# Kernel tuning notes

Hardware: AMD Instinct MI355X
Metric: run time of the kernel (lower is better)

The kernel has to match this reference:

```python
import jax, jax.numpy as jnp
import numpy as np

FREQ_BANDS = 10
LN_EPS = 1e-5


def nerf_positional_encoding(x, L=FREQ_BANDS):
    # x: (..., 3) -> (..., 3*2*L). Per-frequency [sin(2^i x), cos(2^i x)].
    freqs = 2.0 ** jnp.arange(L, dtype=x.dtype)            # (L,)
    xb = x[..., None, :] * freqs[:, None]                  # (..., L, 3)
    enc = jnp.concatenate([jnp.sin(xb), jnp.cos(xb)], -1)  # (..., L, 6)
    return enc.reshape(x.shape[:-1] + (L * 6,))


def farthest_point_sampling(xyz, npoint):
    # xyz: (B, N, 3) -> (B, npoint) int32. Deterministic start at index 0
    # (torch version uses a random start; start choice is arbitrary for FPS).
    B, N, _ = xyz.shape
    binds = jnp.arange(B)

    def step(carry, _):
        dist, far = carry
        c = xyz[binds, far]                                # (B, 3)
        d = jnp.sum((xyz - c[:, None, :]) ** 2, axis=-1)   # (B, N)
        dist = jnp.minimum(dist, d)
        nxt = jnp.argmax(dist, axis=-1).astype(jnp.int32)
        return (dist, nxt), far

    init = (jnp.full((B, N), 1e10, xyz.dtype), jnp.zeros((B,), jnp.int32))
    _, idx = jax.lax.scan(step, init, None, length=npoint)
    return jnp.swapaxes(idx, 0, 1)                         # (B, npoint)


def _layernorm(x, g, b):
    m = jnp.mean(x, axis=-1, keepdims=True)
    v = jnp.var(x, axis=-1, keepdims=True)
    return (x - m) * jax.lax.rsqrt(v + LN_EPS) * g + b


def setup_inputs() -> dict:
    key = jax.random.key(0)
    ks = jax.random.split(key, 8)
    B, N, C = 8, 16384, 64
    d_in = C + 3 * 2 * FREQ_BANDS                          # 124
    dims = [d_in, 128, 128, 256]

    def lin(k, din, dout):
        return jax.random.normal(k, (din, dout), jnp.float32) / np.sqrt(din)

    return {
        "xyz": jax.random.normal(ks[0], (B, N, 3), jnp.float32),
        "features": jax.random.normal(ks[1], (B, N, C), jnp.float32),
        "W1": lin(ks[2], dims[0], dims[1]), "b1": jnp.zeros((dims[1],), jnp.float32),
        "g1": jnp.ones((dims[1],), jnp.float32), "be1": jnp.zeros((dims[1],), jnp.float32),
        "W2": lin(ks[3], dims[1], dims[2]), "b2": jnp.zeros((dims[2],), jnp.float32),
        "g2": jnp.ones((dims[2],), jnp.float32), "be2": jnp.zeros((dims[2],), jnp.float32),
        "W3": lin(ks[4], dims[2], dims[3]), "b3": jnp.zeros((dims[3],), jnp.float32),
        "npoint": 2048,
        "nsample": 32,
    }


def reference(xyz, features, W1, b1, g1, be1, W2, b2, g2, be2, W3, b3, npoint, nsample):
    # FPS centroids
    fps_idx = farthest_point_sampling(xyz, npoint)                 # (B, S)
    new_xyz = jnp.take_along_axis(xyz, fps_idx[..., None], axis=1) # (B, S, 3)

    # KNN: squared distances preserve topk ordering of cdist
    d2 = jnp.sum((new_xyz[:, :, None, :] - xyz[:, None, :, :]) ** 2, axis=-1)  # (B,S,N)
    _, knn_idx = jax.lax.top_k(-d2, nsample)                        # (B, S, k)

    gather = jax.vmap(lambda pts, idx: pts[idx])                    # (N,D),(S,k)->(S,k,D)
    grouped_xyz = gather(xyz, knn_idx)                              # (B, S, k, 3)
    rel_pos = grouped_xyz - new_xyz[:, :, None, :]
    rel_enc = nerf_positional_encoding(rel_pos)                     # (B, S, k, 60)

    grouped_feat = gather(features, knn_idx)                        # (B, S, k, C)
    h = jnp.concatenate([grouped_feat, rel_enc], axis=-1)           # (B, S, k, C+60)

    h = jax.nn.relu(_layernorm(h @ W1 + b1, g1, be1))
    h = jax.nn.relu(_layernorm(h @ W2 + b2, g2, be2))
    h = h @ W3 + b3                                                 # (B, S, k, 256)
    new_features = jnp.max(h, axis=2)                               # (B, S, 256)
    return new_xyz, new_features
```

## Files before the change

kernel.cpp:

```cpp
#include <hip/hip_runtime.h>
#include <cstdint>
#include <cstddef>

#define BATCH   8
#define NPTS    16384
#define CFEAT   64
#define NPOINT  2048
#define NSAMPLE 32
#define DIN     124
#define D1      128
#define D2      128
#define D3      256
#define LN_EPS  1e-5f

#define NFPS      8
#define NBLOCKS   256
#define KNN_ITEMS 128
#define MLP_ITEMS 2048
#define TOT_ITEMS (KNN_ITEMS + MLP_ITEMS)

#define SB_BYTES   19872
#define SMEM_BYTES (8 * SB_BYTES)

#define CTL_QHEAD   0
#define CTL_PROG    1024
#define CTL_KCNT    4096
#define CTL_KFLAG   16384
#define CTL_BYTES   32768

#define PTS16(F) F(0) F(1) F(2) F(3) F(4) F(5) F(6) F(7) \
                 F(8) F(9) F(10) F(11) F(12) F(13) F(14) F(15)

__device__ float          g_sx[BATCH][NPTS];
__device__ float          g_sy[BATCH][NPTS];
__device__ float          g_sz[BATCH][NPTS];
__device__ unsigned short g_so[BATCH][NPTS];

__attribute__((amdgpu_waves_per_eu(4, 4)))
__global__ __launch_bounds__(1024) void fused_kernel(
    const float* __restrict__ xyz, const float* __restrict__ features,
    const float* __restrict__ W1, const float* __restrict__ b1,
    const float* __restrict__ g1, const float* __restrict__ be1,
    const float* __restrict__ W2, const float* __restrict__ b2,
    const float* __restrict__ g2, const float* __restrict__ be2,
    const float* __restrict__ W3, const float* __restrict__ b3,
    int* __restrict__ knn_idx, unsigned char* __restrict__ ctl,
    float* __restrict__ new_xyz, float* __restrict__ out)
{
  __shared__ __align__(16) unsigned char smem[SMEM_BYTES];
  __shared__ unsigned s_item;
  const int t = threadIdx.x;

  unsigned* qhead = (unsigned*)(ctl + CTL_QHEAD);
#define PROG_AT(b)  ((int*)(ctl + CTL_PROG + (b) * 256))
#define KCNT_AT(k)  ((unsigned*)(ctl + CTL_KCNT + (k) * 64))
#define KFLAG_AT(k) ((unsigned*)(ctl + CTL_KFLAG + (k) * 64))

  if (blockIdx.x < NFPS) {
    const int b = blockIdx.x;
    const float* X = xyz + (size_t)b * NPTS * 3;

    float4 (*s_mind4)[1024] = reinterpret_cast<float4(*)[1024]>(smem);
    unsigned short* s_oidx  = (unsigned short*)(smem + 65536);
    float* wvv              = (float*)(smem + 98304);
    unsigned long long* s_packed = (unsigned long long*)(smem + 98368);
    float (*wbb)[6]         = (float(*)[6])(smem + 98496);
    float* gpar             = (float*)(smem + 98944);
    unsigned* cstart        = (unsigned*)(smem + 99008);
    unsigned* ccur          = (unsigned*)(smem + 101120);
    float (*redbuf)[6]      = (float(*)[6])(smem + 103168);

#define DECLP(i) float px##i, py##i, pz##i;
    PTS16(DECLP)
#undef DECLP
#define LOADP(i) { int j = t + (i << 10);  \
    px##i = X[3 * j + 0];                  \
    py##i = X[3 * j + 1];                  \
    pz##i = X[3 * j + 2]; }
    PTS16(LOADP)
#undef LOADP

    {
      float mnx = px0, mxx = px0, mny = py0, mxy = py0, mnz = pz0, mxz = pz0;
#define BB(i) { mnx = fminf(mnx, px##i); mxx = fmaxf(mxx, px##i);  \
                mny = fminf(mny, py##i); mxy = fmaxf(mxy, py##i);  \
                mnz = fminf(mnz, pz##i); mxz = fmaxf(mxz, pz##i); }
      PTS16(BB)
#undef BB
#pragma unroll
      for (int off = 32; off >= 1; off >>= 1) {
        mnx = fminf(mnx, __shfl_xor(mnx, off)); mxx = fmaxf(mxx, __shfl_xor(mxx, off));
        mny = fminf(mny, __shfl_xor(mny, off)); mxy = fmaxf(mxy, __shfl_xor(mxy, off));
        mnz = fminf(mnz, __shfl_xor(mnz, off)); mxz = fmaxf(mxz, __shfl_xor(mxz, off));
      }
      if ((t & 63) == 0) {
        int w = t >> 6;
        redbuf[w][0] = mnx; redbuf[w][1] = mxx; redbuf[w][2] = mny;
        redbuf[w][3] = mxy; redbuf[w][4] = mnz; redbuf[w][5] = mxz;
      }
      if (t < 513) cstart[t] = 0;
      __syncthreads();
      if (t == 0) {
        float a0 = redbuf[0][0], a1 = redbuf[0][1], a2 = redbuf[0][2];
        float a3 = redbuf[0][3], a4 = redbuf[0][4], a5 = redbuf[0][5];
        for (int w = 1; w < 16; ++w) {
          a0 = fminf(a0, redbuf[w][0]); a1 = fmaxf(a1, redbuf[w][1]);
          a2 = fminf(a2, redbuf[w][2]); a3 = fmaxf(a3, redbuf[w][3]);
          a4 = fminf(a4, redbuf[w][4]); a5 = fmaxf(a5, redbuf[w][5]);
        }
        float rx = a1 - a0, ry = a3 - a2, rz = a5 - a4;
        gpar[0] = a0; gpar[1] = a2; gpar[2] = a4;
        gpar[3] = (rx > 1e-20f) ? 8.0f / rx : 0.f;
        gpar[4] = (ry > 1e-20f) ? 8.0f / ry : 0.f;
        gpar[5] = (rz > 1e-20f) ? 8.0f / rz : 0.f;
        s_packed[0] = 0ull; s_packed[1] = 0ull;
      }
      __syncthreads();
    }

#define CELLM(x, y, z) ({                                              \
    int ix_ = (int)((x - gpar[0]) * gpar[3]);                          \
    int iy_ = (int)((y - gpar[1]) * gpar[4]);                          \
    int iz_ = (int)((z - gpar[2]) * gpar[5]);                          \
    ix_ = ix_ < 0 ? 0 : (ix_ > 7 ? 7 : ix_);                           \
    iy_ = iy_ < 0 ? 0 : (iy_ > 7 ? 7 : iy_);                           \
    iz_ = iz_ < 0 ? 0 : (iz_ > 7 ? 7 : iz_);                           \
    (((ix_ & 1) | ((ix_ & 2) << 2) | ((ix_ & 4) << 4))                 \
     | (((iy_ & 1) | ((iy_ & 2) << 2) | ((iy_ & 4) << 4)) << 1)        \
     | (((iz_ & 1) | ((iz_ & 2) << 2) | ((iz_ & 4) << 4)) << 2)); })

#define CIDK(i) { int m_ = CELLM(px##i, py##i, pz##i); \
    atomicAdd(&cstart[m_ + 1], 1u); }
    PTS16(CIDK)
#undef CIDK
    __syncthreads();

    if (t < 64) {
      unsigned v[8], p[8];
      unsigned run = 0;
#pragma unroll
      for (int j = 0; j < 8; ++j) { v[j] = cstart[t * 8 + 1 + j]; run += v[j]; p[j] = run; }
      unsigned tot = run;
#pragma unroll
      for (int off = 1; off < 64; off <<= 1) {
        unsigned u = __shfl_up(run, off);
        if ((t & 63) >= off) run += u;
      }
      unsigned excl = run - tot;
      if (t == 0) cstart[0] = 0;
#pragma unroll
      for (int j = 0; j < 8; ++j) cstart[t * 8 + 1 + j] = excl + p[j];
    }
    __syncthreads();
    if (t < 512) ccur[t] = cstart[t];
    __syncthreads();

#define SCATK(i) { int j = t + (i << 10);                              \
    int m_ = CELLM(px##i, py##i, pz##i);                               \
    unsigned dst = atomicAdd(&ccur[m_], 1u);                           \
    g_sx[b][dst] = px##i; g_sy[b][dst] = py##i; g_sz[b][dst] = pz##i;  \
    g_so[b][dst] = (unsigned short)j; }
    PTS16(SCATK)
#undef SCATK
#undef CELLM
    __syncthreads();

    float tlx = 1e30f, thx = -1e30f, tly = 1e30f, thy = -1e30f,
          tlz = 1e30f, thz = -1e30f;
#define RELK(i) { int p_ = (t << 4) + i;                               \
    px##i = g_sx[b][p_]; py##i = g_sy[b][p_]; pz##i = g_sz[b][p_];     \
    s_oidx[(i << 10) + t] = g_so[b][p_];                               \
    tlx = fminf(tlx, px##i); thx = fmaxf(thx, px##i);                  \
    tly = fminf(tly, py##i); thy = fmaxf(thy, py##i);                  \
    tlz = fminf(tlz, pz##i); thz = fmaxf(thz, pz##i); }
    PTS16(RELK)
#undef RELK
    s_mind4[0][t] = make_float4(1e10f, 1e10f, 1e10f, 1e10f);
    s_mind4[1][t] = make_float4(1e10f, 1e10f, 1e10f, 1e10f);
    s_mind4[2][t] = make_float4(1e10f, 1e10f, 1e10f, 1e10f);
    s_mind4[3][t] = make_float4(1e10f, 1e10f, 1e10f, 1e10f);

#pragma unroll
    for (int off = 32; off >= 1; off >>= 1) {
      tlx = fminf(tlx, __shfl_xor(tlx, off)); thx = fmaxf(thx, __shfl_xor(thx, off));
      tly = fminf(tly, __shfl_xor(tly, off)); thy = fmaxf(thy, __shfl_xor(thy, off));
      tlz = fminf(tlz, __shfl_xor(tlz, off)); thz = fmaxf(thz, __shfl_xor(thz, off));
    }
    if ((t & 63) == 0) {
      int w = t >> 6;
      wbb[w][0] = tlx; wbb[w][1] = thx; wbb[w][2] = tly;
      wbb[w][3] = thy; wbb[w][4] = tlz; wbb[w][5] = thz;
    }

    float mybest = -1.0f;
    float wvmax  = 1e10f;
    float cx = X[0], cy = X[1], cz = X[2];
    __syncthreads();

    for (int s = 0; s < NPOINT; ++s) {
      if (t == 0) {
        float* o = new_xyz + ((size_t)b * NPOINT + s) * 3;
        o[0] = cx; o[1] = cy; o[2] = cz;
        if (((s + 1) & 15) == 0) {
          __builtin_amdgcn_fence(__ATOMIC_RELEASE, "agent");
          __hip_atomic_store(PROG_AT(b), s + 1, __ATOMIC_RELAXED,
                             __HIP_MEMORY_SCOPE_AGENT);
        }
      }
      if (s == NPOINT - 1) break;

      asm volatile("" : "+v"(px0), "+v"(px1), "+v"(px2), "+v"(px3),
                        "+v"(px4), "+v"(px5), "+v"(px6), "+v"(px7),
                        "+v"(px8), "+v"(px9), "+v"(px10), "+v"(px11),
                        "+v"(px12), "+v"(px13), "+v"(px14), "+v"(px15));
      asm volatile("" : "+v"(py0), "+v"(py1), "+v"(py2), "+v"(py3),
                        "+v"(py4), "+v"(py5), "+v"(py6), "+v"(py7),
                        "+v"(py8), "+v"(py9), "+v"(py10), "+v"(py11),
                        "+v"(py12), "+v"(py13), "+v"(py14), "+v"(py15));
      asm volatile("" : "+v"(pz0), "+v"(pz1), "+v"(pz2), "+v"(pz3),
                        "+v"(pz4), "+v"(pz5), "+v"(pz6), "+v"(pz7),
                        "+v"(pz8), "+v"(pz9), "+v"(pz10), "+v"(pz11),
                        "+v"(pz12), "+v"(pz13), "+v"(pz14), "+v"(pz15));

      {
        const int w = t >> 6;
        float lox = wbb[w][0], hix = wbb[w][1];
        float loy = wbb[w][2], hiy = wbb[w][3];
        float loz = wbb[w][4], hiz = wbb[w][5];
        float ddx = fmaxf(fmaxf(lox - cx, cx - hix), 0.f);
        float ddy = fmaxf(fmaxf(loy - cy, cy - hiy), 0.f);
        float ddz = fmaxf(fmaxf(loz - cz, cz - hiz), 0.f);
        float dlb2 = ddx * ddx + ddy * ddy + ddz * ddz;
        if (dlb2 < wvmax * 1.0001f) {
          mybest = -1.0f;
#define DIST(i) ({                                                       \
    float dx_ = __fsub_rn(px##i, cx);                                    \
    float dy_ = __fsub_rn(py##i, cy);                                    \
    float dz_ = __fsub_rn(pz##i, cz);                                    \
    __fadd_rn(__fadd_rn(__fmul_rn(dx_, dx_), __fmul_rn(dy_, dy_)),       \
              __fmul_rn(dz_, dz_)); })
#define PACKSTEP(p, i0, i1, i2, i3) {                                    \
    float4 dv = s_mind4[p][t];                                           \
    dv.x = fminf(dv.x, DIST(i0));                                        \
    dv.y = fminf(dv.y, DIST(i1));                                        \
    dv.z = fminf(dv.z, DIST(i2));                                        \
    dv.w = fminf(dv.w, DIST(i3));                                        \
    s_mind4[p][t] = dv;                                                  \
    mybest = fmaxf(mybest, fmaxf(fmaxf(dv.x, dv.y), fmaxf(dv.z, dv.w))); }
          PACKSTEP(0, 0, 1, 2, 3)
          PACKSTEP(1, 4, 5, 6, 7)
          PACKSTEP(2, 8, 9, 10, 11)
          PACKSTEP(3, 12, 13, 14, 15)
#undef PACKSTEP
#undef DIST
          float wmax = mybest;
#pragma unroll
          for (int off = 32; off >= 1; off >>= 1)
            wmax = fmaxf(wmax, __shfl_xor(wmax, off));
          wvmax = wmax;
          if ((t & 63) == 0) wvv[w] = wmax;
        }
      }
      __syncthreads();

      if (t == 0) s_packed[(s & 1) ^ 1] = 0ull;

      float4 v0 = *(const float4*)&wvv[0];
      float4 v1 = *(const float4*)&wvv[4];
      float4 v2 = *(const float4*)&wvv[8];
      float4 v3 = *(const float4*)&wvv[12];
      float g = fmaxf(
          fmaxf(fmaxf(fmaxf(v0.x, v0.y), fmaxf(v0.z, v0.w)),
                fmaxf(fmaxf(v1.x, v1.y), fmaxf(v1.z, v1.w))),
          fmaxf(fmaxf(fmaxf(v2.x, v2.y), fmaxf(v2.z, v2.w)),
                fmaxf(fmaxf(v3.x, v3.y), fmaxf(v3.z, v3.w))));

      if (mybest == g) {
        unsigned bo = 0xFFFFu;
#pragma unroll
        for (int p = 0; p < 4; ++p) {
          float4 dv = s_mind4[p][t];
          { unsigned o = s_oidx[((4 * p + 0) << 10) + t];
            if (dv.x == g && o < bo) bo = o; }
          { unsigned o = s_oidx[((4 * p + 1) << 10) + t];
            if (dv.y == g && o < bo) bo = o; }
          { unsigned o = s_oidx[((4 * p + 2) << 10) + t];
            if (dv.z == g && o < bo) bo = o; }
          { unsigned o = s_oidx[((4 * p + 3) << 10) + t];
            if (dv.w == g && o < bo) bo = o; }
        }
        unsigned long long pk =
            ((unsigned long long)__float_as_uint(g) << 32) |
            (unsigned)(~bo & 0xFFFFu);
        atomicMax(&s_packed[s & 1], pk);
      }
      __syncthreads();

      unsigned long long gp = s_packed[s & 1];
      int orig = (int)((~(unsigned)(gp & 0xffffffffull)) & 0xFFFFu);
      const float* Wp = X + 3 * (size_t)orig;
      cx = Wp[0]; cy = Wp[1]; cz = Wp[2];
    }
    return;
  }

  for (;;) {
    __syncthreads();
    if (t == 0)
      s_item = __hip_atomic_fetch_add(qhead, 1u, __ATOMIC_RELAXED,
                                      __HIP_MEMORY_SCOPE_AGENT);
    __syncthreads();
    unsigned item = s_item;
    if (item >= TOT_ITEMS) return;

    if (item < KNN_ITEMS) {
      const int k = (int)item;
      const int b = k >> 4;
      const int chunk = k & 15;
      const int lane = t & 63;
      const int wid  = t >> 6;
      const int gidbase = b * NPOINT + chunk * 128 + wid * 8;
      const int need = chunk * 128 + wid * 8 + 8;
      const float* X = xyz + (size_t)b * NPTS * 3;

      if (lane == 0) {
        while (__hip_atomic_load(PROG_AT(b), __ATOMIC_RELAXED,
                                 __HIP_MEMORY_SCOPE_AGENT) < need)
          __builtin_amdgcn_s_sleep(64);
      }
      __builtin_amdgcn_fence(__ATOMIC_ACQUIRE, "agent");

      float cx[8], cy[8], cz[8];
#pragma unroll
      for (int c = 0; c < 8; ++c) {
        const float* p = new_xyz + (size_t)(gidbase + c) * 3;
        cx[c] = p[0]; cy[c] = p[1]; cz[c] = p[2];
      }
      float qd[8]; int qi[8]; float T[8];
#pragma unroll
      for (int c = 0; c < 8; ++c) { qd[c] = 3.4e38f; qi[c] = 0; T[c] = 3.4e38f; }

      for (int base = 0; base < NPTS; base += 64) {
        const int j = base + lane;
        const float x = X[3 * j + 0];
        const float y = X[3 * j + 1];
        const float z = X[3 * j + 2];
#pragma unroll
        for (int c = 0; c < 8; ++c) {
          float dx = __fsub_rn(x, cx[c]);
          float dy = __fsub_rn(y, cy[c]);
          float dz = __fsub_rn(z, cz[c]);
          float v  = __fadd_rn(__fadd_rn(__fmul_rn(dx, dx), __fmul_rn(dy, dy)),
                               __fmul_rn(dz, dz));
          unsigned long long m = __ballot(v < T[c]);
          while (m) {
            int bit = __ffsll(m) - 1;
            m &= m - 1;
            float vb = __shfl(v, bit);
            if (vb < T[c]) {
              int   jb = base + bit;
              float du = __shfl_up(qd[c], 1);
              int   iu = __shfl_up(qi[c], 1);
              bool c2 = (lane > 0) && (vb < du);
              bool c1 = vb < qd[c];
              qd[c] = c2 ? du : (c1 ? vb : qd[c]);
              qi[c] = c2 ? iu : (c1 ? jb : qi[c]);
              T[c] = __shfl(qd[c], 31);
            }
          }
        }
      }
#pragma unroll
      for (int c = 0; c < 8; ++c) {
        if (lane < 32) knn_idx[(size_t)(gidbase + c) * NSAMPLE + lane] = qi[c];
      }
      __builtin_amdgcn_fence(__ATOMIC_RELEASE, "agent");
      if (lane == 0) {
        unsigned d = __hip_atomic_fetch_add(KCNT_AT(k), 1u, __ATOMIC_ACQ_REL,
                                            __HIP_MEMORY_SCOPE_AGENT);
        if (d == 15u)
          __hip_atomic_store(KFLAG_AT(k), 1u, __ATOMIC_RELEASE,
                             __HIP_MEMORY_SCOPE_AGENT);
      }
    } else {
      const int m = (int)(item - KNN_ITEMS);
      const int gbase = m << 3;
      const int b = gbase / NPOINT;
      const int sb = t >> 7;
      const int t127 = t & 127;
      const int g = gbase + sb;

      if (t == 0) {
        while (__hip_atomic_load(KFLAG_AT(m >> 4), __ATOMIC_RELAXED,
                                 __HIP_MEMORY_SCOPE_AGENT) == 0u)
          __builtin_amdgcn_s_sleep(64);
      }
      __syncthreads();
      __builtin_amdgcn_fence(__ATOMIC_ACQUIRE, "agent");

      unsigned char* base_ = smem + sb * SB_BYTES;
      float* bufT = (float*)base_;
      float (*red)[4][2] = (float(*)[4][2])(base_ + 18432);
      float (*lnp)[2]    = (float(*)[2])(base_ + 19456);
      int*   ki          = (int*)(base_ + 19712);
      float* cen         = (float*)(base_ + 19840);

      if (t127 < 32) ki[t127] = knn_idx[(size_t)g * NSAMPLE + t127];
      if (t127 < 3)  cen[t127] = new_xyz[(size_t)g * 3 + t127];
      __syncthreads();

      {
        int r = t127 & 31, cs = (t127 >> 5) << 4;
        const float* frow = features + ((size_t)b * NPTS + ki[r]) * CFEAT + cs;
#pragma unroll
        for (int u = 0; u < 4; ++u) {
          float4 f = *(const float4*)(frow + 4 * u);
          bufT[(cs + 4 * u + 0) * 36 + r] = f.x;
          bufT[(cs + 4 * u + 1) * 36 + r] = f.y;
          bufT[(cs + 4 * u + 2) * 36 + r] = f.z;
          bufT[(cs + 4 * u + 3) * 36 + r] = f.w;
        }
      }
      if (t127 < 32) {
        const float* p = xyz + ((size_t)b * NPTS + ki[t127]) * 3;
        float rx = p[0] - cen[0];
        float ry = p[1] - cen[1];
        float rz = p[2] - cen[2];
#pragma unroll
        for (int l = 0; l < 10; ++l) {
          float sc = (float)(1 << l);
          float ax = rx * sc, ay = ry * sc, az = rz * sc;
          int bbi = (64 + l * 6) * 36 + t127;
          bufT[bbi + 0 * 36] = __sinf(ax);
          bufT[bbi + 1 * 36] = __sinf(ay);
          bufT[bbi + 2 * 36] = __sinf(az);
          bufT[bbi + 3 * 36] = __cosf(ax);
          bufT[bbi + 4 * 36] = __cosf(ay);
          bufT[bbi + 5 * 36] = __cosf(az);
        }
      }
      __syncthreads();

      float acc[32];
      {
        float bias = b1[t127];
#pragma unroll
        for (int r = 0; r < 32; ++r) acc[r] = bias;
        for (int i = 0; i < DIN; ++i) {
          float w = W1[i * D1 + t127];
          const float* hr = &bufT[i * 36];
#pragma unroll
          for (int r = 0; r < 32; ++r) acc[r] = fmaf(hr[r], w, acc[r]);
        }
      }
      {
        __syncthreads();
#pragma unroll
        for (int r = 0; r < 32; ++r) bufT[t127 * 36 + r] = acc[r];
        __syncthreads();
        {
          int r = t127 & 31, seg = t127 >> 5;
          float s = 0.f, ss = 0.f;
#pragma unroll
          for (int u = 0; u < 32; ++u) {
            float v = bufT[(seg * 32 + u) * 36 + r];
            s += v; ss = fmaf(v, v, ss);
          }
          red[r][seg][0] = s; red[r][seg][1] = ss;
        }
        __syncthreads();
        if (t127 < 32) {
          float s  = red[t127][0][0] + red[t127][1][0] + red[t127][2][0] + red[t127][3][0];
          float ss = red[t127][0][1] + red[t127][1][1] + red[t127][2][1] + red[t127][3][1];
          float mm = s * (1.0f / D1);
          float var = ss * (1.0f / D1) - mm * mm;
          lnp[t127][0] = mm;
          lnp[t127][1] = rsqrtf(var + LN_EPS);
        }
        __syncthreads();
        float gg = g1[t127], bb = be1[t127];
#pragma unroll
        for (int r = 0; r < 32; ++r) {
          float v = (acc[r] - lnp[r][0]) * lnp[r][1];
          v = fmaf(v, gg, bb);
          bufT[t127 * 36 + r] = fmaxf(v, 0.f);
        }
        __syncthreads();
      }
      {
        float bias = b2[t127];
#pragma unroll
        for (int r = 0; r < 32; ++r) acc[r] = bias;
        for (int i = 0; i < D1; ++i) {
          float w = W2[i * D2 + t127];
          const float* hr = &bufT[i * 36];
#pragma unroll
          for (int r = 0; r < 32; ++r) acc[r] = fmaf(hr[r], w, acc[r]);
        }
      }
      {
        __syncthreads();
#pragma unroll
        for (int r = 0; r < 32; ++r) bufT[t127 * 36 + r] = acc[r];
        __syncthreads();
        {
          int r = t127 & 31, seg = t127 >> 5;
          float s = 0.f, ss = 0.f;
#pragma unroll
          for (int u = 0; u < 32; ++u) {
            float v = bufT[(seg * 32 + u) * 36 + r];
            s += v; ss = fmaf(v, v, ss);
          }
          red[r][seg][0] = s; red[r][seg][1] = ss;
        }
        __syncthreads();
        if (t127 < 32) {
          float s  = red[t127][0][0] + red[t127][1][0] + red[t127][2][0] + red[t127][3][0];
          float ss = red[t127][0][1] + red[t127][1][1] + red[t127][2][1] + red[t127][3][1];
          float mm = s * (1.0f / D2);
          float var = ss * (1.0f / D2) - mm * mm;
          lnp[t127][0] = mm;
          lnp[t127][1] = rsqrtf(var + LN_EPS);
        }
        __syncthreads();
        float gg = g2[t127], bb = be2[t127];
#pragma unroll
        for (int r = 0; r < 32; ++r) {
          float v = (acc[r] - lnp[r][0]) * lnp[r][1];
          v = fmaf(v, gg, bb);
          bufT[t127 * 36 + r] = fmaxf(v, 0.f);
        }
        __syncthreads();
      }
      float* of = out + (size_t)g * D3;
#pragma unroll 1
      for (int half = 0; half < 2; ++half) {
        int col = t127 + (half << 7);
        float a[32];
        float bias = b3[col];
#pragma unroll
        for (int r = 0; r < 32; ++r) a[r] = bias;
        for (int i = 0; i < D2; ++i) {
          float w = W3[i * D3 + col];
          const float* hr = &bufT[i * 36];
#pragma unroll
          for (int r = 0; r < 32; ++r) a[r] = fmaf(hr[r], w, a[r]);
        }
        float m0 = a[0];
#pragma unroll
        for (int r = 1; r < 32; ++r) m0 = fmaxf(m0, a[r]);
        of[col] = m0;
      }
      __syncthreads();
    }
  }
#undef PROG_AT
#undef KCNT_AT
#undef KFLAG_AT
}

extern "C" void kernel_launch(void* const* d_in, const int* in_sizes, int n_in,
                              void* d_out, int out_size, void* d_ws, size_t ws_size,
                              hipStream_t stream) {
  const float* xyz      = (const float*)d_in[0];
  const float* features = (const float*)d_in[1];
  const float* W1  = (const float*)d_in[2];
  const float* b1  = (const float*)d_in[3];
  const float* g1  = (const float*)d_in[4];
  const float* be1 = (const float*)d_in[5];
  const float* W2  = (const float*)d_in[6];
  const float* b2  = (const float*)d_in[7];
  const float* g2  = (const float*)d_in[8];
  const float* be2 = (const float*)d_in[9];
  const float* W3  = (const float*)d_in[10];
  const float* b3  = (const float*)d_in[11];

  float* new_xyz  = (float*)d_out;
  float* new_feat = (float*)d_out + (size_t)BATCH * NPOINT * 3;

  int* knn_idx = (int*)d_ws;
  unsigned char* ctl = (unsigned char*)d_ws +
                       (size_t)BATCH * NPOINT * NSAMPLE * 4;

  hipMemsetAsync(ctl, 0, CTL_BYTES, stream);
  fused_kernel<<<dim3(NBLOCKS), dim3(1024), 0, stream>>>(
      xyz, features, W1, b1, g1, be1, W2, b2, g2, be2, W3, b3,
      knn_idx, ctl, new_xyz, new_feat);
}
```

Baseline: 4.378 ms.

## Fuse FPS argmax into per-wave packed reduction with single barrier per step

The farthest point sampling loop now computes each wave's packed (distance, index) key inside the wave using shuffles and has one lane atomically max it into a triple-buffered shared slot. This removes one of the two block barriers per iteration and the extra pass over the global maximum. Skipped waves reuse their cached packed key. Rotating three slots lets the next slot be cleared safely without a second barrier, at the cost of a 64-bit shuffle reduction in every active wave.

```diff
diff --git a/kernel.cpp b/kernel.cpp
--- a/kernel.cpp
+++ b/kernel.cpp
@@ -62,8 +62,7 @@
 
     float4 (*s_mind4)[1024] = reinterpret_cast<float4(*)[1024]>(smem);
     unsigned short* s_oidx  = (unsigned short*)(smem + 65536);
-    float* wvv              = (float*)(smem + 98304);
-    unsigned long long* s_packed = (unsigned long long*)(smem + 98368);
+    unsigned long long* slots = (unsigned long long*)(smem + 98304);
     float (*wbb)[6]         = (float(*)[6])(smem + 98496);
     float* gpar             = (float*)(smem + 98944);
     unsigned* cstart        = (unsigned*)(smem + 99008);
@@ -113,7 +112,7 @@
         gpar[3] = (rx > 1e-20f) ? 8.0f / rx : 0.f;
         gpar[4] = (ry > 1e-20f) ? 8.0f / ry : 0.f;
         gpar[5] = (rz > 1e-20f) ? 8.0f / rz : 0.f;
-        s_packed[0] = 0ull; s_packed[1] = 0ull;
+        slots[0] = 0ull; slots[1] = 0ull; slots[2] = 0ull;
       }
       __syncthreads();
     }
@@ -192,8 +191,8 @@
       wbb[w][3] = thy; wbb[w][4] = tlz; wbb[w][5] = thz;
     }
 
-    float mybest = -1.0f;
-    float wvmax  = 1e10f;
+    float wvmax = 1e10f;
+    unsigned long long wpk = 0ull;
     float cx = X[0], cy = X[1], cz = X[2];
     __syncthreads();
 
@@ -232,7 +231,7 @@
         float ddz = fmaxf(fmaxf(loz - cz, cz - hiz), 0.f);
         float dlb2 = ddx * ddx + ddy * ddy + ddz * ddz;
         if (dlb2 < wvmax * 1.0001f) {
-          mybest = -1.0f;
+          float mybest = -1.0f;
 #define DIST(i) ({                                                       \
     float dx_ = __fsub_rn(px##i, cx);                                    \
     float dy_ = __fsub_rn(py##i, cy);                                    \
@@ -258,45 +257,37 @@
           for (int off = 32; off >= 1; off >>= 1)
             wmax = fmaxf(wmax, __shfl_xor(wmax, off));
           wvmax = wmax;
-          if ((t & 63) == 0) wvv[w] = wmax;
-        }
-      }
-      __syncthreads();
-
-      if (t == 0) s_packed[(s & 1) ^ 1] = 0ull;
-
-      float4 v0 = *(const float4*)&wvv[0];
-      float4 v1 = *(const float4*)&wvv[4];
-      float4 v2 = *(const float4*)&wvv[8];
-      float4 v3 = *(const float4*)&wvv[12];
-      float g = fmaxf(
-          fmaxf(fmaxf(fmaxf(v0.x, v0.y), fmaxf(v0.z, v0.w)),
-                fmaxf(fmaxf(v1.x, v1.y), fmaxf(v1.z, v1.w))),
-          fmaxf(fmaxf(fmaxf(v2.x, v2.y), fmaxf(v2.z, v2.w)),
-                fmaxf(fmaxf(v3.x, v3.y), fmaxf(v3.z, v3.w))));
-
-      if (mybest == g) {
-        unsigned bo = 0xFFFFu;
-#pragma unroll
-        for (int p = 0; p < 4; ++p) {
-          float4 dv = s_mind4[p][t];
-          { unsigned o = s_oidx[((4 * p + 0) << 10) + t];
-            if (dv.x == g && o < bo) bo = o; }
-          { unsigned o = s_oidx[((4 * p + 1) << 10) + t];
-            if (dv.y == g && o < bo) bo = o; }
-          { unsigned o = s_oidx[((4 * p + 2) << 10) + t];
-            if (dv.z == g && o < bo) bo = o; }
-          { unsigned o = s_oidx[((4 * p + 3) << 10) + t];
-            if (dv.w == g && o < bo) bo = o; }
-        }
-        unsigned long long pk =
-            ((unsigned long long)__float_as_uint(g) << 32) |
-            (unsigned)(~bo & 0xFFFFu);
-        atomicMax(&s_packed[s & 1], pk);
-      }
-      __syncthreads();
-
-      unsigned long long gp = s_packed[s & 1];
+          unsigned long long pk = 0ull;
+          if (mybest == wmax) {
+            unsigned bo = 0xFFFFu;
+#pragma unroll
+            for (int p = 0; p < 4; ++p) {
+              float4 dv = s_mind4[p][t];
+              { unsigned o = s_oidx[((4 * p + 0) << 10) + t];
+                if (dv.x == wmax && o < bo) bo = o; }
+              { unsigned o = s_oidx[((4 * p + 1) << 10) + t];
+                if (dv.y == wmax && o < bo) bo = o; }
+              { unsigned o = s_oidx[((4 * p + 2) << 10) + t];
+                if (dv.z == wmax && o < bo) bo = o; }
+              { unsigned o = s_oidx[((4 * p + 3) << 10) + t];
+                if (dv.w == wmax && o < bo) bo = o; }
+            }
+            pk = ((unsigned long long)__float_as_uint(wmax) << 32) |
+                 (unsigned)(~bo & 0xFFFFu);
+          }
+#pragma unroll
+          for (int off = 32; off >= 1; off >>= 1) {
+            unsigned long long o = __shfl_xor(pk, off);
+            if (o > pk) pk = o;
+          }
+          wpk = pk;
+        }
+        if ((t & 63) == 0) atomicMax(&slots[s % 3], wpk);
+      }
+      if (t == 0) slots[(s + 1) % 3] = 0ull;
+      __syncthreads();
+
+      unsigned long long gp = slots[s % 3];
       int orig = (int)((~(unsigned)(gp & 0xffffffffull)) & 0xFFFFu);
       const float* Wp = X + 3 * (size_t)orig;
       cx = Wp[0]; cy = Wp[1]; cz = Wp[2];
```

After: 4.938 ms. 1.13x slower.
